# Kernel tuning notes

Measured on AMD Instinct MI355X. Metric: run time of the kernel, lower is better.

The kernel has to match this reference:

```python
import jax, jax.numpy as jnp
from jax import lax
import numpy as np

EPS = 1e-5
CH = [16, 64, 512]


def _conv(x, w, stride):
    # x: [B,D,H,W,Cin], w: [3,3,3,Cin,Cout], centered kernel (padding 1) like ME kernel_size=3
    return lax.conv_general_dilated(
        x, w, (stride, stride, stride), [(1, 1)] * 3,
        dimension_numbers=('NDHWC', 'DHWIO', 'NDHWC'))


def _bn_elu(x, m, gamma, beta):
    # BatchNorm over ACTIVE sites only (ME stores features only at active coords), training-mode stats.
    mm = m[..., None]
    cnt = jnp.sum(m)
    mean = jnp.sum(x * mm, axis=(0, 1, 2, 3)) / cnt
    var = jnp.sum(jnp.square(x - mean) * mm, axis=(0, 1, 2, 3)) / cnt
    xh = (x - mean) * lax.rsqrt(var + EPS) * gamma + beta
    return jax.nn.elu(xh) * mm


def _pool_mask(m):
    # ME stride-2 conv output coords = unique(in_coord // 2) -> OR over 2x2x2 blocks
    return lax.reduce_window(m, 0.0, lax.max, (1, 2, 2, 2), (1, 2, 2, 2), 'VALID')


def _block(x, m_in, wa, ga, ba, wb, gb, bb):
    m_out = _pool_mask(m_in)
    y = _conv(x, wa, 2) * m_out[..., None]   # strided sparse conv, masked to output coords
    y = _bn_elu(y, m_out, ga, ba)
    y = _conv(y, wb, 1) * m_out[..., None]   # stride-1 conv keeps coordinate set
    y = _bn_elu(y, m_out, gb, bb)
    return y, m_out


def setup_inputs() -> dict:
    key = jax.random.key(0)
    ks = jax.random.split(key, 16)
    B, G = 4, 128
    x = jax.random.normal(ks[0], (B, G, G, G, 1), dtype=jnp.float32)
    mask = jax.random.randint(ks[1], (B, G, G, G), 0, 2, dtype=jnp.int32)

    def kconv(k, cin, cout):
        std = np.sqrt(2.0 / (27 * cout))  # kaiming_normal_ fan_out, relu
        return jax.random.normal(k, (3, 3, 3, cin, cout), dtype=jnp.float32) * std

    inp = {'x': x, 'mask': mask,
           'w1a': kconv(ks[2], 1, CH[0]),  'g1a': jnp.ones((CH[0],)), 'b1a': jnp.zeros((CH[0],)),
           'w1b': kconv(ks[3], CH[0], CH[0]), 'g1b': jnp.ones((CH[0],)), 'b1b': jnp.zeros((CH[0],)),
           'w2a': kconv(ks[4], CH[0], CH[1]), 'g2a': jnp.ones((CH[1],)), 'b2a': jnp.zeros((CH[1],)),
           'w2b': kconv(ks[5], CH[1], CH[1]), 'g2b': jnp.ones((CH[1],)), 'b2b': jnp.zeros((CH[1],)),
           'w3a': kconv(ks[6], CH[1], CH[2]), 'g3a': jnp.ones((CH[2],)), 'b3a': jnp.zeros((CH[2],)),
           'w3b': kconv(ks[7], CH[2], CH[2]), 'g3b': jnp.ones((CH[2],)), 'b3b': jnp.zeros((CH[2],)),
           'wm': jax.random.normal(ks[8], (CH[2], CH[2]), dtype=jnp.float32) / np.sqrt(CH[2]),
           'bm': jnp.zeros((CH[2],)),
           'wv': jax.random.normal(ks[9], (CH[2], CH[2]), dtype=jnp.float32) / np.sqrt(CH[2]),
           'bv': jnp.zeros((CH[2],))}
    return inp


def reference(x, mask, w1a, g1a, b1a, w1b, g1b, b1b,
              w2a, g2a, b2a, w2b, g2b, b2b,
              w3a, g3a, b3a, w3b, g3b, b3b,
              wm, bm, wv, bv):
    m0 = mask.astype(jnp.float32)
    h = x * m0[..., None]  # features exist only at active coordinates
    h, m1 = _block(h, m0, w1a, g1a, b1a, w1b, g1b, b1b)
    h, m2 = _block(h, m1, w2a, g2a, b2a, w2b, g2b, b2b)
    h, m3 = _block(h, m2, w3a, g3a, b3a, w3b, g3b, b3b)
    # MinkowskiGlobalPooling: per-batch mean over active sites -> [B, 512]
    denom = jnp.sum(m3, axis=(1, 2, 3), keepdims=False)[:, None]
    pooled = jnp.sum(h * m3[..., None], axis=(1, 2, 3)) / denom
    mean = pooled @ wm + bm
    log_var = pooled @ wv + bv
    return mean, log_var
```

## Files before the change

kernel.cpp:

```cpp
#include <hip/hip_runtime.h>
#include <cstddef>


#define EPSV 1e-5f

typedef _Float16 f16x4 __attribute__((ext_vector_type(4)));
typedef _Float16 f16x8 __attribute__((ext_vector_type(8)));
typedef float f32x4 __attribute__((ext_vector_type(4)));

template <int KC> struct FragSel;
template <> struct FragSel<32> { using T = f16x8; };
template <> struct FragSel<16> { using T = f16x4; };

__device__ __forceinline__ f32x4 mfma16(f16x8 a, f16x8 b, f32x4 c) {
    return __builtin_amdgcn_mfma_f32_16x16x32_f16(a, b, c, 0, 0, 0);
}
__device__ __forceinline__ f32x4 mfma16(f16x4 a, f16x4 b, f32x4 c) {
    return __builtin_amdgcn_mfma_f32_16x16x16f16(a, b, c, 0, 0, 0);
}

__device__ __forceinline__ void gld16(const void* g, void* l) {
    __builtin_amdgcn_global_load_lds(
        (const __attribute__((address_space(1))) unsigned int*)g,
        (__attribute__((address_space(3))) unsigned int*)l, 16, 0, 0);
}

__device__ __forceinline__ int swz(int b) { return b ^ ((b >> 3) & 0x70); }

__global__ __launch_bounds__(256) void pool0_kernel(const int* __restrict__ mask,
                                                    float* __restrict__ mout,
                                                    float* __restrict__ cnt_total) {
    int voxel = blockIdx.x * 256 + threadIdx.x;
    int wo = voxel & 63, ho = (voxel >> 6) & 63, dd = (voxel >> 12) & 63, b = voxel >> 18;
    int any = 0;
#pragma unroll
    for (int dz = 0; dz < 2; ++dz)
#pragma unroll
        for (int hy = 0; hy < 2; ++hy)
#pragma unroll
            for (int wx = 0; wx < 2; ++wx) {
                size_t idx = ((size_t)((b * 128 + 2 * dd + dz) * 128 + 2 * ho + hy)) * 128
                             + 2 * wo + wx;
                any |= mask[idx];
            }
    float mv = any ? 1.f : 0.f;
    mout[voxel] = mv;
    __shared__ float red[256];
    red[threadIdx.x] = mv;
    __syncthreads();
    for (int st = 128; st > 0; st >>= 1) {
        if (threadIdx.x < st) red[threadIdx.x] += red[threadIdx.x + st];
        __syncthreads();
    }
    if (threadIdx.x == 0) atomicAdd(cnt_total, red[0]);
}

__global__ __launch_bounds__(256) void poolf_kernel(const float* __restrict__ min_,
                                                    float* __restrict__ mout,
                                                    int Nout, int lnout,
                                                    float* __restrict__ cnt_total,
                                                    float* __restrict__ cnt_batch) {
    int voxel = blockIdx.x * 256 + threadIdx.x;
    int Nin = Nout * 2;
    int wo = voxel & (Nout - 1);
    int ho = (voxel >> lnout) & (Nout - 1);
    int dd = (voxel >> (2 * lnout)) & (Nout - 1);
    int b = voxel >> (3 * lnout);
    float mx = 0.f;
#pragma unroll
    for (int dz = 0; dz < 2; ++dz)
#pragma unroll
        for (int hy = 0; hy < 2; ++hy)
#pragma unroll
            for (int wx = 0; wx < 2; ++wx) {
                size_t idx = ((size_t)((b * Nin + 2 * dd + dz) * Nin + 2 * ho + hy)) * Nin
                             + 2 * wo + wx;
                mx = fmaxf(mx, min_[idx]);
            }
    mout[voxel] = mx;
    __shared__ float red[256];
    red[threadIdx.x] = mx;
    __syncthreads();
    for (int st = 128; st > 0; st >>= 1) {
        if (threadIdx.x < st) red[threadIdx.x] += red[threadIdx.x + st];
        __syncthreads();
    }
    if (threadIdx.x == 0) {
        atomicAdd(cnt_total, red[0]);
        if (cnt_batch) atomicAdd(&cnt_batch[b], red[0]);
    }
}

__global__ __launch_bounds__(256) void wtrans_all(
    const float* __restrict__ w1b, const float* __restrict__ w2a,
    const float* __restrict__ w2b, const float* __restrict__ w3a,
    const float* __restrict__ w3b,
    _Float16* __restrict__ o1b, _Float16* __restrict__ o2a,
    _Float16* __restrict__ o2b, _Float16* __restrict__ o3a,
    _Float16* __restrict__ o3b) {
    __shared__ float tile[32][33];
    int bid = blockIdx.x;
    const float* W; _Float16* O; int CIN, COUT, rel, TCO;
    if (bid < 27)        { W = w1b; O = o1b; CIN = 16;  COUT = 16;  rel = bid;        TCO = 1; }
    else if (bid < 81)   { W = w2a; O = o2a; CIN = 16;  COUT = 64;  rel = bid - 27;   TCO = 2; }
    else if (bid < 189)  { W = w2b; O = o2b; CIN = 64;  COUT = 64;  rel = bid - 81;   TCO = 2; }
    else if (bid < 1053) { W = w3a; O = o3a; CIN = 64;  COUT = 512; rel = bid - 189;  TCO = 16; }
    else                 { W = w3b; O = o3b; CIN = 512; COUT = 512; rel = bid - 1053; TCO = 16; }
    int TCI = (CIN + 31) >> 5;
    int per_t = TCI * TCO;
    int t = rel / per_t;
    int rr = rel - t * per_t;
    int tci = rr / TCO, tco = rr - tci * TCO;
    int ci0 = tci * 32, co0 = tco * 32;
    int tid = threadIdx.x;
    int c32 = tid & 31, r8 = tid >> 5;
#pragma unroll
    for (int j = 0; j < 4; ++j) {
        int ci = ci0 + j * 8 + r8, co = co0 + c32;
        if (ci < CIN && co < COUT)
            tile[j * 8 + r8][c32] = W[((size_t)t * CIN + ci) * COUT + co];
    }
    __syncthreads();
#pragma unroll
    for (int j = 0; j < 4; ++j) {
        int co = co0 + j * 8 + r8, ci = ci0 + c32;
        if (co < COUT && ci < CIN)
            O[((size_t)t * COUT + co) * CIN + ci] = (_Float16)tile[c32][j * 8 + r8];
    }
}

__global__ __launch_bounds__(256) void conv1a_kernel(const float* __restrict__ x,
                                                     const int* __restrict__ mask,
                                                     const float* __restrict__ w,
                                                     const float* __restrict__ m1,
                                                     _Float16* __restrict__ out,
                                                     float* __restrict__ stats) {
    int voxel = blockIdx.x * 256 + threadIdx.x;
    int wo = voxel & 63, ho = (voxel >> 6) & 63, dd = (voxel >> 12) & 63, b = voxel >> 18;
    float acc[16];
#pragma unroll
    for (int i = 0; i < 16; ++i) acc[i] = 0.f;
    for (int kd = 0; kd < 3; ++kd) {
        int id = 2 * dd + kd - 1;
        if ((unsigned)id >= 128u) continue;
        for (int kh = 0; kh < 3; ++kh) {
            int ih = 2 * ho + kh - 1;
            if ((unsigned)ih >= 128u) continue;
            for (int kw = 0; kw < 3; ++kw) {
                int iw = 2 * wo + kw - 1;
                if ((unsigned)iw >= 128u) continue;
                size_t idx = ((size_t)((b * 128 + id) * 128 + ih)) * 128 + iw;
                float xv = x[idx] * (float)mask[idx];
                const float* wp = w + ((kd * 3 + kh) * 3 + kw) * 16;
#pragma unroll
                for (int co = 0; co < 16; ++co) acc[co] = fmaf(xv, wp[co], acc[co]);
            }
        }
    }
    float m = m1[voxel];
    _Float16* op = out + (size_t)voxel * 16;
    __shared__ float red[256 * 32];
#pragma unroll
    for (int co = 0; co < 16; ++co) {
        float v = acc[co] * m;
        op[co] = (_Float16)v;
        red[threadIdx.x * 32 + co] = v;
        red[threadIdx.x * 32 + 16 + co] = v * v;
    }
    __syncthreads();
    for (int st = 128; st > 0; st >>= 1) {
        if (threadIdx.x < st) {
#pragma unroll
            for (int k = 0; k < 32; ++k)
                red[threadIdx.x * 32 + k] += red[(threadIdx.x + st) * 32 + k];
        }
        __syncthreads();
    }
    if (threadIdx.x < 32) {
        float* sb = stats + (blockIdx.x & 7) * 32;
        atomicAdd(&sb[threadIdx.x], red[threadIdx.x]);
    }
}

template <int CIN, int COUT, int NTILE, int STRIDE, int NIN, int NOUT,
          int TW, int LTW, int TH, int LTH, int TD, int WM, int MINW, int TAPG,
          bool STATS>
__global__ __launch_bounds__(256, MINW) void conv_mfma(const _Float16* __restrict__ in,
                                                       const _Float16* __restrict__ wt,
                                                       const float* __restrict__ mout,
                                                       _Float16* __restrict__ out,
                                                       const _Float16* __restrict__ zbuf,
                                                       float* __restrict__ stats) {
    constexpr int M = TW * TH * TD;
    constexpr int KC = (CIN >= 32) ? 32 : 16;
    constexpr int KB = KC * 2;
    constexpr int LKB = (KC >= 32) ? 6 : 5;
    constexpr int HW_ = (TW - 1) * STRIDE + 3;
    constexpr int HH_ = (TH - 1) * STRIDE + 3;
    constexpr int HD_ = (TD - 1) * STRIDE + 3;
    constexpr int HV = HW_ * HH_ * HD_;
    constexpr int LPV = KB / 16;
    constexpr int VPI = 64 / LPV;
    constexpr int NIH = (HV + VPI - 1) / VPI;
    constexpr int HVP = NIH * VPI;
    constexpr int WN = 4 / WM;
    constexpr int WMT = M / WM;
    constexpr int WNT = NTILE / WN;
    constexpr int NAF = WMT / 16;
    constexpr int NBF = WNT / 16;
    constexpr int NBLK = COUT / NTILE;
    constexpr int NTW = NOUT / TW, NTH = NOUT / TH, NTD = NOUT / TD;
    constexpr int NUMM = 4 * NTW * NTH * NTD;
    constexpr int BI = (NTILE * KB + 1023) / 1024;
    constexpr int NG = 27 / TAPG;
    constexpr int BTAP = NTILE * KB;

    using Frag = typename FragSel<KC>::T;

    __shared__ _Float16 halo[HVP * KC];
    __shared__ _Float16 bbuf[2 * TAPG * NTILE * KC];

    int cpx = gridDim.x >> 3;
    int bid = (blockIdx.x & 7) * cpx + (blockIdx.x >> 3);

    int nblk = (NBLK > 1) ? bid / NUMM : 0;
    int mblk = (NBLK > 1) ? bid % NUMM : bid;
    int tw = mblk % NTW;
    int th = (mblk / NTW) % NTH;
    int td = (mblk / (NTW * NTH)) % NTD;
    int b = mblk / (NTW * NTH * NTD);
    int d0 = td * TD * STRIDE - 1, h0 = th * TH * STRIDE - 1, w0 = tw * TW * STRIDE - 1;

    int tid = threadIdx.x;
    int wv = tid >> 6, lane = tid & 63, m16 = lane & 15, quad = lane >> 4;
    int wm_ = wv % WM, wn_ = wv / WM;
    int qb = quad * (KB / 4);

    int abase_b[NAF];
#pragma unroll
    for (int r = 0; r < NAF; ++r) {
        int vloc = wm_ * WMT + r * 16 + m16;
        int vw = vloc & (TW - 1), vh = (vloc >> LTW) & (TH - 1), vd = vloc >> (LTW + LTH);
        int avox = ((vd * STRIDE) * HH_ + vh * STRIDE) * HW_ + vw * STRIDE;
        abase_b[r] = avox * KB + qb;
    }
    int bofsw[NBF];
#pragma unroll
    for (int f = 0; f < NBF; ++f)
        bofsw[f] = swz((wn_ * WNT + f * 16 + m16) * KB + qb);

    int bsrc[2];
    bool bok[2];
#pragma unroll
    for (int k = 0; k < 2; ++k) {
        int i = wv + 4 * k;
        int S = i * 1024 + lane * 16;
        int Bq = swz(S);
        int row = Bq >> LKB;
        int cb = Bq & (KB - 1);
        bsrc[k] = row * CIN + (cb >> 1);
        bok[k] = (i < BI) && ((BTAP % 1024 == 0) || (row < NTILE));
    }

    f32x4 acc[NAF][NBF];
#pragma unroll
    for (int r = 0; r < NAF; ++r)
#pragma unroll
        for (int f = 0; f < NBF; ++f) acc[r][f] = (f32x4){0.f, 0.f, 0.f, 0.f};

    auto stage_halo = [&](int c0) {
        for (int i = wv; i < NIH; i += 4) {
            int S = i * 1024 + lane * 16;
            int Bq = swz(S);
            int hv = Bq >> LKB;
            int cb = Bq & (KB - 1);
            int hw = hv % HW_;
            int t2 = hv / HW_;
            int hh = t2 % HH_;
            int hd = t2 / HH_;
            int d = d0 + hd, h = h0 + hh, w = w0 + hw;
            bool ok = (hv < HV) && ((unsigned)d < (unsigned)NIN) &&
                      ((unsigned)h < (unsigned)NIN) && ((unsigned)w < (unsigned)NIN);
            const _Float16* g =
                ok ? in + ((size_t)(((b * NIN + d) * NIN + h) * NIN + w)) * CIN + c0 + (cb >> 1)
                   : zbuf;
            gld16(g, (char*)halo + i * 1024);
        }
    };

    auto stage_B = [&](int tap, int jslot, int c0) {
        const _Float16* wb = wt + (size_t)tap * (COUT * CIN) + (size_t)nblk * NTILE * CIN + c0;
#pragma unroll
        for (int k = 0; k < 2; ++k) {
            if (bok[k])
                gld16(wb + bsrc[k], (char*)bbuf + (size_t)jslot * BTAP + (wv + 4 * k) * 1024);
        }
    };

    for (int c0 = 0; c0 < CIN; c0 += KC) {
        __syncthreads();
        stage_halo(c0);
#pragma unroll
        for (int j = 0; j < TAPG; ++j) stage_B(j, j, c0);

        for (int g = 0; g < NG; ++g) {
            __syncthreads();
            if (g + 1 < NG) {
                int tb2 = (g + 1) * TAPG;
                int js = ((g + 1) & 1) * TAPG;
#pragma unroll
                for (int j = 0; j < TAPG; ++j) stage_B(tb2 + j, js + j, c0);
            }
            int tb = g * TAPG;
            int kd = tb / 9, rr = tb - kd * 9, kh = rr / 3, kw = rr - kh * 3;
            int tvb = ((kd * HH_ + kh) * HW_ + kw) * KB;
            const char* bp = (const char*)bbuf + (size_t)((g & 1) * TAPG) * BTAP;
            __builtin_amdgcn_s_setprio(1);
#pragma unroll
            for (int j = 0; j < TAPG; ++j) {
                Frag a[NAF], bb[NBF];
#pragma unroll
                for (int r = 0; r < NAF; ++r)
                    a[r] = *(const Frag*)((const char*)halo + swz(abase_b[r] + tvb + j * KB));
#pragma unroll
                for (int f = 0; f < NBF; ++f)
                    bb[f] = *(const Frag*)(bp + (size_t)j * BTAP + bofsw[f]);
#pragma unroll
                for (int r = 0; r < NAF; ++r)
#pragma unroll
                    for (int f = 0; f < NBF; ++f) acc[r][f] = mfma16(a[r], bb[f], acc[r][f]);
            }
            __builtin_amdgcn_s_setprio(0);
        }
    }

    int n0 = nblk * NTILE + wn_ * WNT + m16;
    float sv[NBF], qv[NBF];
    if constexpr (STATS) {
#pragma unroll
        for (int f = 0; f < NBF; ++f) { sv[f] = 0.f; qv[f] = 0.f; }
    }
#pragma unroll
    for (int r = 0; r < NAF; ++r) {
#pragma unroll
        for (int j = 0; j < 4; ++j) {
            int vloc = wm_ * WMT + r * 16 + quad * 4 + j;
            int vw = vloc & (TW - 1), vh = (vloc >> LTW) & (TH - 1), vd = vloc >> (LTW + LTH);
            int od = td * TD + vd, oh = th * TH + vh, ow = tw * TW + vw;
            size_t gvox = ((size_t)((b * NOUT + od) * NOUT + oh)) * NOUT + ow;
            float mv = mout[gvox];
            _Float16* op = out + gvox * COUT + n0;
#pragma unroll
            for (int f = 0; f < NBF; ++f) {
                float val = acc[r][f][j] * mv;
                op[f * 16] = (_Float16)val;
                if constexpr (STATS) { sv[f] += val; qv[f] += val * val; }
            }
        }
    }
    if constexpr (STATS) {
        float* sb = stats + (blockIdx.x & 7) * (2 * COUT);
#pragma unroll
        for (int f = 0; f < NBF; ++f) {
            float s = sv[f], q = qv[f];
            s += __shfl_xor(s, 16);
            s += __shfl_xor(s, 32);
            q += __shfl_xor(q, 16);
            q += __shfl_xor(q, 32);
            if (lane < 16) {
                int c = n0 + f * 16;
                atomicAdd(&sb[c], s);
                atomicAdd(&sb[COUT + c], q);
            }
        }
    }
}

template <int C, int LOGC>
__global__ __launch_bounds__(256) void bn_apply2(_Float16* __restrict__ x,
                                                 const float* __restrict__ m,
                                                 const float* __restrict__ stats,
                                                 const float* __restrict__ cntp,
                                                 const float* __restrict__ gamma,
                                                 const float* __restrict__ beta, long n) {
    __shared__ float cf[2 * C];
    float cn = *cntp;
    for (int c = threadIdx.x; c < C; c += 256) {
        float s = 0.f, q = 0.f;
#pragma unroll
        for (int k = 0; k < 8; ++k) {
            s += stats[k * 2 * C + c];
            q += stats[k * 2 * C + C + c];
        }
        float mean = s / cn;
        float var = q / cn - mean * mean;
        float sc = rsqrtf(var + EPSV) * gamma[c];
        cf[c] = sc;
        cf[C + c] = beta[c] - mean * sc;
    }
    __syncthreads();
    long stride = (long)gridDim.x * 2048;
    for (long i8 = ((long)blockIdx.x * 256 + threadIdx.x) * 8; i8 < n; i8 += stride) {
        int c = (int)(i8 & (C - 1));
        long v = i8 >> LOGC;
        f16x8 xv = *(const f16x8*)(x + i8);
        float mv = m[v];
        f16x8 o;
#pragma unroll
        for (int k = 0; k < 8; ++k) {
            float xh = (float)xv[k] * cf[c + k] + cf[C + c + k];
            float e = xh > 0.f ? xh : expm1f(xh);
            o[k] = (_Float16)(e * mv);
        }
        *(f16x8*)(x + i8) = o;
    }
}

__global__ __launch_bounds__(256) void gpool_kernel(const _Float16* __restrict__ h,
                                                    const float* __restrict__ m3,
                                                    const float* __restrict__ stats,
                                                    const float* __restrict__ cntp,
                                                    const float* __restrict__ gamma,
                                                    const float* __restrict__ beta,
                                                    float* __restrict__ pooled) {
    __shared__ float cf[1024];
    float cn = *cntp;
    for (int c = threadIdx.x; c < 512; c += 256) {
        float s = 0.f, q = 0.f;
#pragma unroll
        for (int k = 0; k < 8; ++k) {
            s += stats[k * 1024 + c];
            q += stats[k * 1024 + 512 + c];
        }
        float mean = s / cn;
        float var = q / cn - mean * mean;
        float sc = rsqrtf(var + EPSV) * gamma[c];
        cf[c] = sc;
        cf[512 + c] = beta[c] - mean * sc;
    }
    __syncthreads();
    int b = blockIdx.x >> 6, seg = blockIdx.x & 63;
    int ch = (threadIdx.x & 63) * 8;
    int v0 = threadIdx.x >> 6;
    float scl[8], shf[8];
#pragma unroll
    for (int k = 0; k < 8; ++k) {
        scl[k] = cf[ch + k];
        shf[k] = cf[512 + ch + k];
    }
    float s[8];
#pragma unroll
    for (int k = 0; k < 8; ++k) s[k] = 0.f;
    for (int v = v0; v < 64; v += 4) {
        int vox = b * 4096 + seg * 64 + v;
        float mv = m3[vox];
        f16x8 xv = *(const f16x8*)(h + (size_t)vox * 512 + ch);
#pragma unroll
        for (int k = 0; k < 8; ++k) {
            float xh = (float)xv[k] * scl[k] + shf[k];
            float e = xh > 0.f ? xh : expm1f(xh);
            s[k] += e * mv;
        }
    }
#pragma unroll
    for (int k = 0; k < 8; ++k) atomicAdd(&pooled[b * 512 + ch + k], s[k]);
}

__global__ __launch_bounds__(256) void head_kernel(const float* __restrict__ pooled,
                                                   const float* __restrict__ cntb,
                                                   const float* __restrict__ wm,
                                                   const float* __restrict__ bm,
                                                   const float* __restrict__ wv,
                                                   const float* __restrict__ bv,
                                                   float* __restrict__ out) {
    int t = blockIdx.x * 256 + threadIdx.x;
    int which = t >> 11;
    int b = (t >> 9) & 3;
    int j = t & 511;
    const float* W = which ? wv : wm;
    float bias = which ? bv[j] : bm[j];
    const float* p = pooled + b * 512;
    float s = 0.f;
    for (int c = 0; c < 512; ++c) s = fmaf(p[c], W[c * 512 + j], s);
    out[t] = s / cntb[b] + bias;
}

extern "C" void kernel_launch(void* const* d_in, const int* in_sizes, int n_in,
                              void* d_out, int out_size, void* d_ws, size_t ws_size,
                              hipStream_t stream) {
    const float* x   = (const float*)d_in[0];
    const int* mask  = (const int*)d_in[1];
    const float* w1a = (const float*)d_in[2];
    const float* g1a = (const float*)d_in[3];
    const float* b1a = (const float*)d_in[4];
    const float* w1b = (const float*)d_in[5];
    const float* g1b = (const float*)d_in[6];
    const float* b1b = (const float*)d_in[7];
    const float* w2a = (const float*)d_in[8];
    const float* g2a = (const float*)d_in[9];
    const float* b2a = (const float*)d_in[10];
    const float* w2b = (const float*)d_in[11];
    const float* g2b = (const float*)d_in[12];
    const float* b2b = (const float*)d_in[13];
    const float* w3a = (const float*)d_in[14];
    const float* g3a = (const float*)d_in[15];
    const float* b3a = (const float*)d_in[16];
    const float* w3b = (const float*)d_in[17];
    const float* g3b = (const float*)d_in[18];
    const float* b3b = (const float*)d_in[19];
    const float* wm  = (const float*)d_in[20];
    const float* bm  = (const float*)d_in[21];
    const float* wv  = (const float*)d_in[22];
    const float* bv  = (const float*)d_in[23];
    float* out = (float*)d_out;

    char* ws = (char*)d_ws;
    _Float16* A  = (_Float16*)(ws + 0);
    _Float16* Bb = (_Float16*)(ws + 33554432);
    _Float16* w1bh = (_Float16*)(ws + 67108864);
    _Float16* w2ah = (_Float16*)(ws + 67125248);
    _Float16* w2bh = (_Float16*)(ws + 67182592);
    _Float16* w3ah = (_Float16*)(ws + 67403776);
    _Float16* w3bh = (_Float16*)(ws + 69173248);
    float* m1 = (float*)(ws + 83329024);
    float* m2 = (float*)(ws + 87523328);
    float* m3 = (float*)(ws + 88047616);
    float* counts = (float*)(ws + 88113152);
    float* stats  = (float*)(ws + 88113216);
    float* pooled = (float*)(ws + 88309824);
    _Float16* zbuf = (_Float16*)(ws + 88318016);

    float* sL0 = stats;
    float* sL1 = stats + 1 * 8192;
    float* sL2 = stats + 2 * 8192;
    float* sL3 = stats + 3 * 8192;
    float* sL4 = stats + 4 * 8192;
    float* sL5 = stats + 5 * 8192;

    _Float16* h1a = A;
    _Float16* h1b = Bb;
    _Float16* h2a = A;
    _Float16* h2b = Bb;
    _Float16* h3a = A;
    _Float16* h3b = Bb;

    hipMemsetAsync(counts, 0, 64 + 196608 + 8192 + 256, stream);

    pool0_kernel<<<4096, 256, 0, stream>>>(mask, m1, counts + 0);
    poolf_kernel<<<512, 256, 0, stream>>>(m1, m2, 32, 5, counts + 1, nullptr);
    poolf_kernel<<<64, 256, 0, stream>>>(m2, m3, 16, 4, counts + 2, counts + 4);

    wtrans_all<<<7965, 256, 0, stream>>>(w1b, w2a, w2b, w3a, w3b,
                                         w1bh, w2ah, w2bh, w3ah, w3bh);

    conv1a_kernel<<<4096, 256, 0, stream>>>(x, mask, w1a, m1, h1a, sL0);
    bn_apply2<16, 4><<<2048, 256, 0, stream>>>(h1a, m1, sL0, counts + 0, g1a, b1a, 16777216L);

    conv_mfma<16, 16, 16, 1, 64, 64, 8, 3, 4, 2, 4, 4, 6, 3, true>
        <<<8192, 256, 0, stream>>>(h1a, w1bh, m1, h1b, zbuf, sL1);
    bn_apply2<16, 4><<<2048, 256, 0, stream>>>(h1b, m1, sL1, counts + 0, g1b, b1b, 16777216L);

    conv_mfma<16, 64, 64, 2, 64, 32, 4, 2, 4, 2, 4, 2, 4, 3, true>
        <<<2048, 256, 0, stream>>>(h1b, w2ah, m2, h2a, zbuf, sL2);
    bn_apply2<64, 6><<<1024, 256, 0, stream>>>(h2a, m2, sL2, counts + 1, g2a, b2a, 8388608L);

    conv_mfma<64, 64, 64, 1, 32, 32, 8, 3, 4, 2, 4, 2, 3, 3, true>
        <<<1024, 256, 0, stream>>>(h2a, w2bh, m2, h2b, zbuf, sL3);
    bn_apply2<64, 6><<<1024, 256, 0, stream>>>(h2b, m2, sL3, counts + 1, g2b, b2b, 8388608L);

    conv_mfma<64, 512, 64, 2, 32, 16, 4, 2, 4, 2, 4, 2, 2, 3, true>
        <<<2048, 256, 0, stream>>>(h2b, w3ah, m3, h3a, zbuf, sL4);
    bn_apply2<512, 9><<<512, 256, 0, stream>>>(h3a, m3, sL4, counts + 2, g3a, b3a, 8388608L);

    conv_mfma<512, 512, 128, 1, 16, 16, 8, 3, 4, 2, 4, 2, 2, 3, true>
        <<<512, 256, 0, stream>>>(h3a, w3bh, m3, h3b, zbuf, sL5);

    gpool_kernel<<<256, 256, 0, stream>>>(h3b, m3, sL5, counts + 2, g3b, b3b, pooled);
    head_kernel<<<16, 256, 0, stream>>>(pooled, counts + 4, wm, bm, wv, bv, out);
}
```

Baseline: 989.0 us.

## Fuse BN+ELU of level-1 activations into conv halo staging

Adds a FUSEIN mode to conv_mfma that computes BN scale/shift from the accumulated stats and applies normalization, ELU and masking while loading the input halo into LDS. Two bn_apply2 passes over the largest (64^3, 16-channel) tensors are dropped. The first stride-1 conv's tile is also enlarged from 8x4x4 to 8x8x8 with fewer blocks and lower min-waves. In exchange, staging now uses synchronous register loads plus expm1f per element instead of async global_load_lds, and halo voxels are normalized repeatedly across overlapping tiles.

Result: faster. 867.0 us (-12.3%).

```diff
diff --git a/kernel.cpp b/kernel.cpp
--- a/kernel.cpp
+++ b/kernel.cpp
@@ -184,13 +184,18 @@
 
 template <int CIN, int COUT, int NTILE, int STRIDE, int NIN, int NOUT,
           int TW, int LTW, int TH, int LTH, int TD, int WM, int MINW, int TAPG,
-          bool STATS>
+          bool STATS, bool FUSEIN>
 __global__ __launch_bounds__(256, MINW) void conv_mfma(const _Float16* __restrict__ in,
                                                        const _Float16* __restrict__ wt,
                                                        const float* __restrict__ mout,
                                                        _Float16* __restrict__ out,
                                                        const _Float16* __restrict__ zbuf,
-                                                       float* __restrict__ stats) {
+                                                       float* __restrict__ stats,
+                                                       const float* __restrict__ min_,
+                                                       const float* __restrict__ statsi,
+                                                       const float* __restrict__ cnti,
+                                                       const float* __restrict__ gin,
+                                                       const float* __restrict__ bin) {
     constexpr int M = TW * TH * TD;
     constexpr int KC = (CIN >= 32) ? 32 : 16;
     constexpr int KB = KC * 2;
@@ -214,11 +219,13 @@
     constexpr int BI = (NTILE * KB + 1023) / 1024;
     constexpr int NG = 27 / TAPG;
     constexpr int BTAP = NTILE * KB;
+    static_assert(!FUSEIN || CIN == KC, "FUSEIN requires single K-chunk");
 
     using Frag = typename FragSel<KC>::T;
 
     __shared__ _Float16 halo[HVP * KC];
     __shared__ _Float16 bbuf[2 * TAPG * NTILE * KC];
+    __shared__ float cfs[FUSEIN ? 2 * CIN : 2];
 
     int cpx = gridDim.x >> 3;
     int bid = (blockIdx.x & 7) * cpx + (blockIdx.x >> 3);
@@ -235,6 +242,23 @@
     int wv = tid >> 6, lane = tid & 63, m16 = lane & 15, quad = lane >> 4;
     int wm_ = wv % WM, wn_ = wv / WM;
     int qb = quad * (KB / 4);
+
+    if constexpr (FUSEIN) {
+        float cn = *cnti;
+        for (int c = tid; c < CIN; c += 256) {
+            float s = 0.f, q = 0.f;
+#pragma unroll
+            for (int k = 0; k < 8; ++k) {
+                s += statsi[k * 2 * CIN + c];
+                q += statsi[k * 2 * CIN + CIN + c];
+            }
+            float mean = s / cn;
+            float var = q / cn - mean * mean;
+            float sc = rsqrtf(var + EPSV) * gin[c];
+            cfs[c] = sc;
+            cfs[CIN + c] = bin[c] - mean * sc;
+        }
+    }
 
     int abase_b[NAF];
 #pragma unroll
@@ -281,10 +305,28 @@
             int d = d0 + hd, h = h0 + hh, w = w0 + hw;
             bool ok = (hv < HV) && ((unsigned)d < (unsigned)NIN) &&
                       ((unsigned)h < (unsigned)NIN) && ((unsigned)w < (unsigned)NIN);
-            const _Float16* g =
-                ok ? in + ((size_t)(((b * NIN + d) * NIN + h) * NIN + w)) * CIN + c0 + (cb >> 1)
-                   : zbuf;
-            gld16(g, (char*)halo + i * 1024);
+            if constexpr (FUSEIN) {
+                f16x8 o = (f16x8){0, 0, 0, 0, 0, 0, 0, 0};
+                if (ok) {
+                    size_t gvox = ((size_t)(((b * NIN + d) * NIN + h) * NIN + w));
+                    f16x8 xv = *(const f16x8*)(in + gvox * CIN + (cb >> 1));
+                    float mv = min_[gvox];
+                    int cc = cb >> 1;
+#pragma unroll
+                    for (int k = 0; k < 8; ++k) {
+                        float xh = (float)xv[k] * cfs[cc + k] + cfs[CIN + cc + k];
+                        float e = xh > 0.f ? xh : expm1f(xh);
+                        o[k] = (_Float16)(e * mv);
+                    }
+                }
+                *(f16x8*)((char*)halo + S) = o;
+            } else {
+                const _Float16* g =
+                    ok ? in + ((size_t)(((b * NIN + d) * NIN + h) * NIN + w)) * CIN + c0
+                             + (cb >> 1)
+                       : zbuf;
+                gld16(g, (char*)halo + i * 1024);
+            }
         }
     };
 
@@ -554,26 +596,29 @@
                                          w1bh, w2ah, w2bh, w3ah, w3bh);
 
     conv1a_kernel<<<4096, 256, 0, stream>>>(x, mask, w1a, m1, h1a, sL0);
-    bn_apply2<16, 4><<<2048, 256, 0, stream>>>(h1a, m1, sL0, counts + 0, g1a, b1a, 16777216L);
-
-    conv_mfma<16, 16, 16, 1, 64, 64, 8, 3, 4, 2, 4, 4, 6, 3, true>
-        <<<8192, 256, 0, stream>>>(h1a, w1bh, m1, h1b, zbuf, sL1);
-    bn_apply2<16, 4><<<2048, 256, 0, stream>>>(h1b, m1, sL1, counts + 0, g1b, b1b, 16777216L);
-
-    conv_mfma<16, 64, 64, 2, 64, 32, 4, 2, 4, 2, 4, 2, 4, 3, true>
-        <<<2048, 256, 0, stream>>>(h1b, w2ah, m2, h2a, zbuf, sL2);
+
+    conv_mfma<16, 16, 16, 1, 64, 64, 8, 3, 8, 3, 8, 4, 4, 3, true, true>
+        <<<2048, 256, 0, stream>>>(h1a, w1bh, m1, h1b, zbuf, sL1,
+                                   m1, sL0, counts + 0, g1a, b1a);
+
+    conv_mfma<16, 64, 64, 2, 64, 32, 4, 2, 4, 2, 4, 2, 4, 3, true, true>
+        <<<2048, 256, 0, stream>>>(h1b, w2ah, m2, h2a, zbuf, sL2,
+                                   m1, sL1, counts + 0, g1b, b1b);
     bn_apply2<64, 6><<<1024, 256, 0, stream>>>(h2a, m2, sL2, counts + 1, g2a, b2a, 8388608L);
 
-    conv_mfma<64, 64, 64, 1, 32, 32, 8, 3, 4, 2, 4, 2, 3, 3, true>
-        <<<1024, 256, 0, stream>>>(h2a, w2bh, m2, h2b, zbuf, sL3);
+    conv_mfma<64, 64, 64, 1, 32, 32, 8, 3, 4, 2, 4, 2, 3, 3, true, false>
+        <<<1024, 256, 0, stream>>>(h2a, w2bh, m2, h2b, zbuf, sL3,
+                                   nullptr, nullptr, nullptr, nullptr, nullptr);
     bn_apply2<64, 6><<<1024, 256, 0, stream>>>(h2b, m2, sL3, counts + 1, g2b, b2b, 8388608L);
 
-    conv_mfma<64, 512, 64, 2, 32, 16, 4, 2, 4, 2, 4, 2, 2, 3, true>
-        <<<2048, 256, 0, stream>>>(h2b, w3ah, m3, h3a, zbuf, sL4);
+    conv_mfma<64, 512, 64, 2, 32, 16, 4, 2, 4, 2, 4, 2, 2, 3, true, false>
+        <<<2048, 256, 0, stream>>>(h2b, w3ah, m3, h3a, zbuf, sL4,
+                                   nullptr, nullptr, nullptr, nullptr, nullptr);
     bn_apply2<512, 9><<<512, 256, 0, stream>>>(h3a, m3, sL4, counts + 2, g3a, b3a, 8388608L);
 
-    conv_mfma<512, 512, 128, 1, 16, 16, 8, 3, 4, 2, 4, 2, 2, 3, true>
-        <<<512, 256, 0, stream>>>(h3a, w3bh, m3, h3b, zbuf, sL5);
+    conv_mfma<512, 512, 128, 1, 16, 16, 8, 3, 4, 2, 4, 2, 2, 3, true, false>
+        <<<512, 256, 0, stream>>>(h3a, w3bh, m3, h3b, zbuf, sL5,
+                                  nullptr, nullptr, nullptr, nullptr, nullptr);
 
     gpool_kernel<<<256, 256, 0, stream>>>(h3b, m3, sL5, counts + 2, g3b, b3b, pooled);
     head_kernel<<<16, 256, 0, stream>>>(pooled, counts + 4, wm, bm, wv, bv, out);
```
